# Kernel tuning notes

Hardware: AMD Instinct MI355X
Metric: run time of the kernel (lower is better)

Reference implementation:

```python
import jax, jax.numpy as jnp
import numpy as np

K_NEIGHBOURS = 16
ITERATIONS = 3
NUM_CLASSES = 20
N_POINTS = 20000


def setup_inputs() -> dict:
    key = jax.random.key(0)
    k1, k2 = jax.random.split(key)
    logits = jax.random.normal(k1, (N_POINTS, NUM_CLASSES), dtype=jnp.float32)
    coords = jax.random.uniform(k2, (N_POINTS, 3), dtype=jnp.float32)
    # nn.init.eye_ then *= -0.1
    compat_w = (-0.1 * jnp.eye(NUM_CLASSES, dtype=jnp.float32))
    return {"logits": logits, "coords": coords, "compat_w": compat_w}


def _knn_graph(coords, k):
    # torch.cdist (p=2): euclidean distances, (N, N)
    sq = jnp.sum(coords * coords, axis=-1)
    d2 = sq[:, None] + sq[None, :] - 2.0 * (coords @ coords.T)
    dists = jnp.sqrt(jnp.clip(d2, 0.0))
    # smallest-k -> top_k of negated distances
    _, idx = jax.lax.top_k(-dists, k)  # (N, k)
    return idx


def reference(logits, coords, compat_w):
    knn_idx = _knn_graph(coords, K_NEIGHBOURS)
    q = jax.nn.softmax(logits, axis=-1)
    for _ in range(ITERATIONS):
        neighbour_q = q[knn_idx]            # (N, k, K) gather
        msg = jnp.mean(neighbour_q, axis=1)  # (N, K)
        refined = logits + msg @ compat_w.T  # nn.Linear: x @ W^T
        q = jax.nn.softmax(refined, axis=-1)
    return (refined, q)
```

## Files before the change

kernel.cpp:

```cpp
#include <hip/hip_runtime.h>

#define N_PTS 20000
#define NCLS 20
#define KNN 16
#define GRID 12
#define NCELLS (GRID * GRID * GRID)
#define HCELL (1.0f / (float)GRID)
#define CAND_CAP 640
#define KEY_CAP 128
#define R_TARGET 0.0680f

__device__ __forceinline__ int cell1d(float v) {
    int c = (int)(v * (float)GRID);
    return min(max(c, 0), GRID - 1);
}

__global__ __launch_bounds__(256) void build_kernel(const float* __restrict__ coords,
                                                    const float* __restrict__ logits,
                                                    int* __restrict__ cellCount,
                                                    int* __restrict__ doneCtr,
                                                    int* __restrict__ readyFlag,
                                                    int* __restrict__ cellStart,
                                                    int* __restrict__ cellCursor,
                                                    float4* __restrict__ sortedPts,
                                                    int* __restrict__ orig,
                                                    float* __restrict__ ls,
                                                    float* __restrict__ q0s) {
    const int p = blockIdx.x * blockDim.x + threadIdx.x;
    const bool act = (p < N_PTS);
    float x = 0.f, y = 0.f, z = 0.f;
    int c = 0;
    if (act) {
        x = coords[3 * p + 0];
        y = coords[3 * p + 1];
        z = coords[3 * p + 2];
        c = (cell1d(z) * GRID + cell1d(y)) * GRID + cell1d(x);
        atomicAdd(&cellCount[c], 1);
    }
    __syncthreads();
    __shared__ bool isLast;
    if (threadIdx.x == 0)
        isLast = (atomicAdd(doneCtr, 1) == (int)gridDim.x - 1);
    __syncthreads();

    if (isLast) {
        __shared__ int part[256];
        const int t = threadIdx.x;
        const int base = t * 7;
        int local[7];
        int s = 0;
#pragma unroll
        for (int i = 0; i < 7; ++i) {
            const int cc = base + i;
            const int v = (cc < NCELLS)
                ? __hip_atomic_load(&cellCount[cc], __ATOMIC_RELAXED, __HIP_MEMORY_SCOPE_AGENT)
                : 0;
            local[i] = s;
            s += v;
        }
        part[t] = s;
        __syncthreads();
        for (int off2 = 1; off2 < 256; off2 <<= 1) {
            const int v = part[t] + ((t >= off2) ? part[t - off2] : 0);
            __syncthreads();
            part[t] = v;
            __syncthreads();
        }
        const int excl = (t > 0) ? part[t - 1] : 0;
#pragma unroll
        for (int i = 0; i < 7; ++i) {
            const int cc = base + i;
            if (cc < NCELLS) {
                cellStart[cc] = excl + local[i];
                __hip_atomic_store(&cellCursor[cc], excl + local[i],
                                   __ATOMIC_RELAXED, __HIP_MEMORY_SCOPE_AGENT);
            }
        }
        if (t == 255) cellStart[NCELLS] = part[255];
        __syncthreads();
        if (t == 0)
            __hip_atomic_store(readyFlag, 1, __ATOMIC_RELAXED, __HIP_MEMORY_SCOPE_AGENT);
    }
    if (threadIdx.x == 0) {
        while (__hip_atomic_load(readyFlag, __ATOMIC_RELAXED, __HIP_MEMORY_SCOPE_AGENT) == 0)
            __builtin_amdgcn_s_sleep(2);
    }
    __syncthreads();
    if (!act) return;

    const int pos = atomicAdd(&cellCursor[c], 1);
    sortedPts[pos] = make_float4(x, y, z, __uint_as_float((unsigned)p));
    orig[pos] = p;
    const float4* l4 = (const float4*)(logits + p * NCLS);
    float v[NCLS];
#pragma unroll
    for (int u = 0; u < 5; ++u) {
        const float4 a = l4[u];
        v[4 * u + 0] = a.x; v[4 * u + 1] = a.y;
        v[4 * u + 2] = a.z; v[4 * u + 3] = a.w;
    }
    float4* d4 = (float4*)(ls + pos * NCLS);
#pragma unroll
    for (int u = 0; u < 5; ++u)
        d4[u] = make_float4(v[4 * u], v[4 * u + 1], v[4 * u + 2], v[4 * u + 3]);
    float mx = v[0];
#pragma unroll
    for (int cc2 = 1; cc2 < NCLS; ++cc2) mx = fmaxf(mx, v[cc2]);
    float sum = 0.f;
#pragma unroll
    for (int cc2 = 0; cc2 < NCLS; ++cc2) { v[cc2] = __expf(v[cc2] - mx); sum += v[cc2]; }
    const float inv = 1.f / sum;
    float4* q4 = (float4*)(q0s + pos * NCLS);
#pragma unroll
    for (int u = 0; u < 5; ++u)
        q4[u] = make_float4(v[4 * u] * inv, v[4 * u + 1] * inv,
                            v[4 * u + 2] * inv, v[4 * u + 3] * inv);
}

__device__ void knn_ladder(const float4* __restrict__ sortedPts,
                           const int* __restrict__ cellStart,
                           const float4 qp, const int s, int hw,
                           unsigned long long* keys, const int lane,
                           int* __restrict__ knn_out) {
    const unsigned long long laneLt = (1ull << lane) - 1ull;
    const int cx = cell1d(qp.x), cy = cell1d(qp.y), cz = cell1d(qp.z);
    float g = 0.9995f * (float)hw * HCELL;
    float tau = g * g;
    int cnt = 0;
    for (int att = 0; att < 16; ++att) {
        cnt = 0;
        const int xlo = max(cx - hw, 0), xhi = min(cx + hw, GRID - 1);
        const int ylo = max(cy - hw, 0), yhi = min(cy + hw, GRID - 1);
        const int zlo = max(cz - hw, 0), zhi = min(cz + hw, GRID - 1);
        for (int zz = zlo; zz <= zhi; ++zz) {
            for (int yy = ylo; yy <= yhi; ++yy) {
                const int rowc = (zz * GRID + yy) * GRID;
                const int beg = cellStart[rowc + xlo];
                const int end = cellStart[rowc + xhi + 1];
                for (int j0 = beg; j0 < end; j0 += 64) {
                    const int j = j0 + lane;
                    const bool jv = j < end;
                    const float4 pt = sortedPts[jv ? j : beg];
                    const float dx = pt.x - qp.x, dy = pt.y - qp.y, dz = pt.z - qp.z;
                    const float d2 = dx * dx + dy * dy + dz * dz;
                    const bool take = jv && (d2 < tau);
                    const unsigned long long mm = __ballot(take);
                    if (take) {
                        const int pos = cnt + (int)__popcll(mm & laneLt);
                        if (pos < KEY_CAP)
                            keys[pos] = (((unsigned long long)__float_as_uint(d2)) << 32) |
                                        (unsigned long long)(unsigned)j;
                    }
                    cnt += (int)__popcll(mm);
                }
            }
        }
        if (cnt >= KNN && cnt <= KEY_CAP) break;
        if (cnt < KNN) {
            if (hw < GRID - 1) { ++hw; g = 0.9995f * (float)hw * HCELL; tau = g * g; }
            else tau *= 2.5f;
        } else {
            tau *= 0.6f;
        }
    }
    const int m = min(cnt, KEY_CAP);
    const unsigned long long k0 = (lane < m) ? keys[lane] : ~0ull;
    const unsigned long long k1 = (lane + 64 < m) ? keys[lane + 64] : ~0ull;
    int r0 = 0, r1 = 0;
    for (int j = 0; j < m; ++j) {
        const unsigned long long kj = keys[j];
        r0 += (kj < k0); r1 += (kj < k1);
    }
    if (lane < m && r0 < KNN)      knn_out[s * KNN + r0] = (int)(unsigned)(k0 & 0xffffffffull);
    if (lane + 64 < m && r1 < KNN) knn_out[s * KNN + r1] = (int)(unsigned)(k1 & 0xffffffffull);
}

__global__ __launch_bounds__(256) void knn_kernel(const float4* __restrict__ sortedPts,
                                                  const int* __restrict__ cellStart,
                                                  int* __restrict__ knn_out) {
    __shared__ float4 cand[CAND_CAP];
    __shared__ unsigned long long keys[4][KEY_CAP];
    const int lane = threadIdx.x & 63;
    const int wave = threadIdx.x >> 6;
    const int c = blockIdx.x;
    const int cz = c / (GRID * GRID);
    const int cy = (c / GRID) % GRID;
    const int cx = c % GRID;
    const int pbeg = cellStart[c];
    const int pend = cellStart[c + 1];
    const int npts = pend - pbeg;
    if (npts <= 0) return;
    const int bd = (cx == 0 || cx == GRID - 1) + (cy == 0 || cy == GRID - 1) +
                   (cz == 0 || cz == GRID - 1);
    const int hs = (bd >= 2) ? 2 : 1;
    const unsigned long long laneLt = (1ull << lane) - 1ull;

    const int xlo = max(cx - hs, 0), xhi = min(cx + hs, GRID - 1);
    const int ylo = max(cy - hs, 0), yhi = min(cy + hs, GRID - 1);
    const int zlo = max(cz - hs, 0), zhi = min(cz + hs, GRID - 1);
    const int ny = yhi - ylo + 1;
    const int nruns = (zhi - zlo + 1) * ny;

    int beg = 0, len = 0;
    if (lane < nruns) {
        const int zz = zlo + lane / ny;
        const int yy = ylo + lane % ny;
        const int rowc = (zz * GRID + yy) * GRID;
        beg = cellStart[rowc + xlo];
        len = cellStart[rowc + xhi + 1] - beg;
    }
    int off = len;
#pragma unroll
    for (int sh = 1; sh < 32; sh <<= 1) {
        const int o = __shfl_up(off, sh, 64);
        if (lane >= sh) off += o;
    }
    const int nc = __shfl(off, nruns - 1);
    off -= len;
    const int ownRun = (cz - zlo) * ny + (cy - ylo);
    const int ownOff = __shfl(off, ownRun) + (pbeg - __shfl(beg, ownRun));

    if (nc <= CAND_CAP) {
        for (int r = wave; r < nruns; r += 4) {
            const int rb = __shfl(beg, r);
            const int rl = __shfl(len, r);
            const int ro = __shfl(off, r);
            for (int i = lane; i < rl; i += 64) {
                float4 pt = sortedPts[rb + i];
                pt.w = __uint_as_float((unsigned)(rb + i));
                cand[ro + i] = pt;
            }
        }
    }
    __syncthreads();

    if (nc > CAND_CAP) {
        for (int idx = wave; idx < npts; idx += 4)
            knn_ladder(sortedPts, cellStart, sortedPts[pbeg + idx], pbeg + idx,
                       hs, keys[wave], lane, knn_out);
        return;
    }

    const float taumaxr = 0.9995f * (float)hs * HCELL;
    const float taumax = taumaxr * taumaxr;

    for (int idx = wave; idx < npts; idx += 4) {
        const int s = pbeg + idx;
        const float4 qp = cand[ownOff + idx];
        float r = R_TARGET;
        const float inv2r = 0.5f / r;
        const float fx = (fminf(qp.x + r, 1.f) - fmaxf(qp.x - r, 0.f)) * inv2r;
        const float fy = (fminf(qp.y + r, 1.f) - fmaxf(qp.y - r, 0.f)) * inv2r;
        const float fz = (fminf(qp.z + r, 1.f) - fmaxf(qp.z - r, 0.f)) * inv2r;
        const float f = fmaxf(fx * fy * fz, 0.05f);
        r = R_TARGET * __powf(f, -0.33333334f);
        float tau = fminf(r * r, taumax);
        bool triedMax = (tau >= taumax * 0.999f);

        int cnt = 0;
        bool ok = false;
        for (int att = 0; att < 5 && !ok; ++att) {
            cnt = 0;
            for (int j0 = 0; j0 < nc; j0 += 64) {
                const int j = j0 + lane;
                float d2 = 1e30f;
                unsigned pw = 0;
                if (j < nc) {
                    const float4 pt = cand[j];
                    const float dx = pt.x - qp.x, dy = pt.y - qp.y, dz = pt.z - qp.z;
                    d2 = dx * dx + dy * dy + dz * dz;
                    pw = __float_as_uint(pt.w);
                }
                const bool take = d2 < tau;
                const unsigned long long mm = __ballot(take);
                if (take) {
                    const int pos = cnt + (int)__popcll(mm & laneLt);
                    if (pos < KEY_CAP)
                        keys[wave][pos] =
                            (((unsigned long long)__float_as_uint(d2)) << 32) |
                            (unsigned long long)pw;
                }
                cnt += (int)__popcll(mm);
            }
            if (cnt >= KNN && cnt <= KEY_CAP) ok = true;
            else if (cnt < KNN) {
                if (triedMax) break;
                tau = taumax; triedMax = true;
            } else tau *= 0.6f;
        }
        if (!ok) {
            knn_ladder(sortedPts, cellStart, qp, s, hs + 1, keys[wave], lane, knn_out);
            continue;
        }
        const int m = cnt;
        const unsigned long long k0 = (lane < m) ? keys[wave][lane] : ~0ull;
        const unsigned long long k1 = (lane + 64 < m) ? keys[wave][lane + 64] : ~0ull;
        int r0 = 0, r1 = 0;
        for (int j = 0; j < m; ++j) {
            const unsigned long long kj = keys[wave][j];
            r0 += (kj < k0); r1 += (kj < k1);
        }
        if (lane < m && r0 < KNN)      knn_out[s * KNN + r0] = (int)(unsigned)(k0 & 0xffffffffull);
        if (lane + 64 < m && r1 < KNN) knn_out[s * KNN + r1] = (int)(unsigned)(k1 & 0xffffffffull);
    }
}

__global__ __launch_bounds__(256) void crf_iter_kernel(const float* __restrict__ ls,
                                                       const float* __restrict__ W,
                                                       const int* __restrict__ knn,
                                                       const float* __restrict__ qin,
                                                       float* __restrict__ qout,
                                                       const int* __restrict__ orig,
                                                       float* __restrict__ outRef,
                                                       float* __restrict__ outQ) {
    __shared__ float Ws[NCLS * NCLS];
    for (int i = threadIdx.x; i < NCLS * NCLS; i += blockDim.x) Ws[i] = W[i];
    __syncthreads();
    const int t = blockIdx.x * blockDim.x + threadIdx.x;
    const int p = t >> 3;
    const int sub = t & 7;
    if (p >= N_PTS) return;

    float acc[NCLS];
#pragma unroll
    for (int c = 0; c < NCLS; ++c) acc[c] = 0.f;

    const int2 k2 = ((const int2*)(knn + p * KNN))[sub];
    const int ids[2] = {k2.x, k2.y};
#pragma unroll
    for (int u = 0; u < 2; ++u) {
        unsigned id = (unsigned)ids[u];
        if (id >= N_PTS) id = 0;
        const float4* r4 = (const float4*)(qin + id * NCLS);
#pragma unroll
        for (int v = 0; v < 5; ++v) {
            const float4 a = r4[v];
            acc[4 * v + 0] += a.x; acc[4 * v + 1] += a.y;
            acc[4 * v + 2] += a.z; acc[4 * v + 3] += a.w;
        }
    }
#pragma unroll
    for (int c = 0; c < NCLS; ++c) {
        acc[c] += __shfl_xor(acc[c], 1, 64);
        acc[c] += __shfl_xor(acc[c], 2, 64);
        acc[c] += __shfl_xor(acc[c], 4, 64);
        acc[c] *= (1.f / 16.f);
    }

    const int c0 = (sub & 3) * 5;
    float ref[5];
#pragma unroll
    for (int i = 0; i < 5; ++i) {
        float s = ls[p * NCLS + c0 + i];
#pragma unroll
        for (int k = 0; k < NCLS; ++k) s += acc[k] * Ws[(c0 + i) * NCLS + k];
        ref[i] = s;
    }

    float mx = ref[0];
#pragma unroll
    for (int i = 1; i < 5; ++i) mx = fmaxf(mx, ref[i]);
    mx = fmaxf(mx, __shfl_xor(mx, 1, 64));
    mx = fmaxf(mx, __shfl_xor(mx, 2, 64));
    float ex[5];
    float ps = 0.f;
#pragma unroll
    for (int i = 0; i < 5; ++i) { ex[i] = __expf(ref[i] - mx); ps += ex[i]; }
    ps += __shfl_xor(ps, 1, 64);
    ps += __shfl_xor(ps, 2, 64);
    const float inv = 1.f / ps;

    if (sub < 4) {
        if (outRef != nullptr) {
            const int o = orig[p];
#pragma unroll
            for (int i = 0; i < 5; ++i) {
                outRef[o * NCLS + c0 + i] = ref[i];
                outQ[o * NCLS + c0 + i] = ex[i] * inv;
            }
        } else {
#pragma unroll
            for (int i = 0; i < 5; ++i) qout[p * NCLS + c0 + i] = ex[i] * inv;
        }
    }
}

extern "C" void kernel_launch(void* const* d_in, const int* in_sizes, int n_in,
                              void* d_out, int out_size, void* d_ws, size_t ws_size,
                              hipStream_t stream) {
    const float* logits = (const float*)d_in[0];
    const float* coords = (const float*)d_in[1];
    const float* W      = (const float*)d_in[2];
    float* out = (float*)d_out;

    char* ws = (char*)d_ws;
    size_t off = 0;
    int* knn = (int*)(ws + off);              off += (size_t)N_PTS * KNN * 4;
    off = (off + 255) & ~(size_t)255;
    float* ls = (float*)(ws + off);           off += (size_t)N_PTS * NCLS * 4;
    off = (off + 255) & ~(size_t)255;
    float* q0s = (float*)(ws + off);          off += (size_t)N_PTS * NCLS * 4;
    off = (off + 255) & ~(size_t)255;
    float4* sortedPts = (float4*)(ws + off);  off += (size_t)N_PTS * 16;
    off = (off + 255) & ~(size_t)255;
    int* orig = (int*)(ws + off);             off += (size_t)N_PTS * 4;
    off = (off + 255) & ~(size_t)255;
    int* cellCount = (int*)(ws + off);        off += (size_t)(NCELLS + 2) * 4;
    int* doneCtr   = cellCount + NCELLS;
    int* readyFlag = cellCount + NCELLS + 1;
    off = (off + 255) & ~(size_t)255;
    int* cellStart = (int*)(ws + off);        off += (size_t)(NCELLS + 1) * 4;
    off = (off + 255) & ~(size_t)255;
    int* cellCursor = (int*)(ws + off);
    float* q1s = out + N_PTS * NCLS;

    const int threads = 256;
    const int pblocks = (N_PTS + threads - 1) / threads;
    const int cblocks = (8 * N_PTS + threads - 1) / threads;

    hipMemsetAsync(cellCount, 0, (NCELLS + 2) * sizeof(int), stream);
    build_kernel<<<pblocks, threads, 0, stream>>>(coords, logits, cellCount, doneCtr,
                                                  readyFlag, cellStart, cellCursor,
                                                  sortedPts, orig, ls, q0s);
    knn_kernel<<<NCELLS, threads, 0, stream>>>(sortedPts, cellStart, knn);
    crf_iter_kernel<<<cblocks, threads, 0, stream>>>(ls, W, knn, q0s, q1s, orig,
                                                     nullptr, nullptr);
    crf_iter_kernel<<<cblocks, threads, 0, stream>>>(ls, W, knn, q1s, q0s, orig,
                                                     nullptr, nullptr);
    crf_iter_kernel<<<cblocks, threads, 0, stream>>>(ls, W, knn, q0s, nullptr, orig,
                                                     out, out + N_PTS * NCLS);
}
```

Before: 125.0 us.

## Process two query points per wavefront using half-wave candidate scans in kNN

The kNN kernel now splits each 64-lane wavefront into two 32-lane halves, each handling its own query point with its own key buffer. Candidate scans step by 32 lanes and use half-wave ballot masks, and ranking covers up to 128 keys with four keys per lane. Failed points are sent to the full-wave ladder fallback one after the other. The aim is better lane use when there are few candidates per cell, at the cost of more loop iterations per point, extra divergence handling and double the shared key storage.

```diff
diff --git a/kernel.cpp b/kernel.cpp
--- a/kernel.cpp
+++ b/kernel.cpp
@@ -179,9 +179,12 @@
                                                   const int* __restrict__ cellStart,
                                                   int* __restrict__ knn_out) {
     __shared__ float4 cand[CAND_CAP];
-    __shared__ unsigned long long keys[4][KEY_CAP];
+    __shared__ unsigned long long keys[8][KEY_CAP];
     const int lane = threadIdx.x & 63;
     const int wave = threadIdx.x >> 6;
+    const int half = lane >> 5;
+    const int hl = lane & 31;
+    const unsigned hlLt = (1u << hl) - 1u;
     const int c = blockIdx.x;
     const int cz = c / (GRID * GRID);
     const int cy = (c / GRID) % GRID;
@@ -237,16 +240,21 @@
     if (nc > CAND_CAP) {
         for (int idx = wave; idx < npts; idx += 4)
             knn_ladder(sortedPts, cellStart, sortedPts[pbeg + idx], pbeg + idx,
-                       hs, keys[wave], lane, knn_out);
+                       hs, keys[wave * 2], lane, knn_out);
         return;
     }
 
     const float taumaxr = 0.9995f * (float)hs * HCELL;
     const float taumax = taumaxr * taumaxr;
-
-    for (int idx = wave; idx < npts; idx += 4) {
+    const int w2 = wave * 2 + half;
+
+    for (int ri = 0;; ++ri) {
+        const int idx = wave * 2 + half + 8 * ri;
+        const bool activeP = idx < npts;
+        if (!__any(activeP)) break;
         const int s = pbeg + idx;
-        const float4 qp = cand[ownOff + idx];
+        const float4 qp = cand[activeP ? (ownOff + idx) : 0];
+
         float r = R_TARGET;
         const float inv2r = 0.5f / r;
         const float fx = (fminf(qp.x + r, 1.f) - fmaxf(qp.x - r, 0.f)) * inv2r;
@@ -258,50 +266,74 @@
         bool triedMax = (tau >= taumax * 0.999f);
 
         int cnt = 0;
-        bool ok = false;
-        for (int att = 0; att < 5 && !ok; ++att) {
-            cnt = 0;
-            for (int j0 = 0; j0 < nc; j0 += 64) {
-                const int j = j0 + lane;
+        bool ok = false, gaveup = false;
+        for (int att = 0; att < 5; ++att) {
+            const bool need = activeP && !ok && !gaveup;
+            if (!__any(need)) break;
+            if (need) cnt = 0;
+            for (int j0 = 0; j0 < nc; j0 += 32) {
+                const int j = j0 + hl;
                 float d2 = 1e30f;
                 unsigned pw = 0;
-                if (j < nc) {
+                if (need && j < nc) {
                     const float4 pt = cand[j];
                     const float dx = pt.x - qp.x, dy = pt.y - qp.y, dz = pt.z - qp.z;
                     d2 = dx * dx + dy * dy + dz * dz;
                     pw = __float_as_uint(pt.w);
                 }
-                const bool take = d2 < tau;
+                const bool take = need && (j < nc) && (d2 < tau);
                 const unsigned long long mm = __ballot(take);
+                const unsigned mh = (unsigned)(mm >> (half * 32));
                 if (take) {
-                    const int pos = cnt + (int)__popcll(mm & laneLt);
+                    const int pos = cnt + (int)__popc(mh & hlLt);
                     if (pos < KEY_CAP)
-                        keys[wave][pos] =
+                        keys[w2][pos] =
                             (((unsigned long long)__float_as_uint(d2)) << 32) |
                             (unsigned long long)pw;
                 }
-                cnt += (int)__popcll(mm);
-            }
-            if (cnt >= KNN && cnt <= KEY_CAP) ok = true;
-            else if (cnt < KNN) {
-                if (triedMax) break;
-                tau = taumax; triedMax = true;
-            } else tau *= 0.6f;
-        }
-        if (!ok) {
-            knn_ladder(sortedPts, cellStart, qp, s, hs + 1, keys[wave], lane, knn_out);
-            continue;
-        }
-        const int m = cnt;
-        const unsigned long long k0 = (lane < m) ? keys[wave][lane] : ~0ull;
-        const unsigned long long k1 = (lane + 64 < m) ? keys[wave][lane + 64] : ~0ull;
-        int r0 = 0, r1 = 0;
-        for (int j = 0; j < m; ++j) {
-            const unsigned long long kj = keys[wave][j];
-            r0 += (kj < k0); r1 += (kj < k1);
-        }
-        if (lane < m && r0 < KNN)      knn_out[s * KNN + r0] = (int)(unsigned)(k0 & 0xffffffffull);
-        if (lane + 64 < m && r1 < KNN) knn_out[s * KNN + r1] = (int)(unsigned)(k1 & 0xffffffffull);
+                if (need) cnt += (int)__popc(mh);
+            }
+            if (need) {
+                if (cnt >= KNN && cnt <= KEY_CAP) ok = true;
+                else if (cnt < KNN) {
+                    if (triedMax) gaveup = true;
+                    else { tau = taumax; triedMax = true; }
+                } else tau *= 0.6f;
+            }
+        }
+
+        if (activeP && ok) {
+            const int m = cnt;
+            unsigned long long kk0, kk1, kk2, kk3;
+            kk0 = (hl       < m) ? keys[w2][hl]       : ~0ull;
+            kk1 = (hl + 32  < m) ? keys[w2][hl + 32]  : ~0ull;
+            kk2 = (hl + 64  < m) ? keys[w2][hl + 64]  : ~0ull;
+            kk3 = (hl + 96  < m) ? keys[w2][hl + 96]  : ~0ull;
+            int rr0 = 0, rr1 = 0, rr2 = 0, rr3 = 0;
+            for (int j = 0; j < m; ++j) {
+                const unsigned long long kj = keys[w2][j];
+                rr0 += (kj < kk0); rr1 += (kj < kk1);
+                rr2 += (kj < kk2); rr3 += (kj < kk3);
+            }
+            if (hl      < m && rr0 < KNN) knn_out[s * KNN + rr0] = (int)(unsigned)(kk0 & 0xffffffffull);
+            if (hl + 32 < m && rr1 < KNN) knn_out[s * KNN + rr1] = (int)(unsigned)(kk1 & 0xffffffffull);
+            if (hl + 64 < m && rr2 < KNN) knn_out[s * KNN + rr2] = (int)(unsigned)(kk2 & 0xffffffffull);
+            if (hl + 96 < m && rr3 < KNN) knn_out[s * KNN + rr3] = (int)(unsigned)(kk3 & 0xffffffffull);
+        }
+
+        const unsigned long long gm = __ballot(activeP && !ok);
+        const bool failA = (gm & 1ull) != 0;
+        const bool failB = ((gm >> 32) & 1ull) != 0;
+        if (failA) {
+            const int ia = wave * 2 + 0 + 8 * ri;
+            knn_ladder(sortedPts, cellStart, cand[ownOff + ia], pbeg + ia,
+                       hs + 1, keys[wave * 2 + 0], lane, knn_out);
+        }
+        if (failB) {
+            const int ib = wave * 2 + 1 + 8 * ri;
+            knn_ladder(sortedPts, cellStart, cand[ownOff + ib], pbeg + ib,
+                       hs + 1, keys[wave * 2 + 1], lane, knn_out);
+        }
     }
 }
 
```

Measured after the change: 125.3 us. Within noise of the previous version (+0.2%).
